# Performance work log

Hardware: AMD Instinct MI355X
Metric: run time of the kernel (lower is better)

Reference implementation:

```python
import jax, jax.numpy as jnp
import numpy as np

B, NCAP, LV, LT, C = 64, 64, 197, 32, 512
NSP = LV - 1          # 196 spatial patches
NUM_KEEP = 98         # ceil(196 * sparse_ratio=0.5)
KEEPED = 49           # int(196 * aggr_ratio=0.5 * sparse_ratio=0.5)
HID = 102             # int(512 * dim_ratio=0.2)
LN_EPS = 1e-5


def _normalize(x):
    # torch F.normalize: x / max(||x||, 1e-12)
    return x / jnp.maximum(jnp.linalg.norm(x, axis=-1, keepdims=True), 1e-12)


def setup_inputs() -> dict:
    key = jax.random.key(0)
    ks = jax.random.split(key, 8)
    def rn(k, shape, s=0.02):
        return jax.random.normal(k, shape, jnp.float32) * s
    return {
        "img_embs": jax.random.normal(ks[0], (B, LV, C), jnp.float32),
        "cap_embs": jax.random.normal(ks[1], (NCAP, LT, C), jnp.float32),
        "cap_lens": jnp.full((NCAP,), LT, jnp.int32),
        "ln_gamma": jnp.ones((C,), jnp.float32),
        "ln_beta": jnp.zeros((C,), jnp.float32),
        "w1": rn(ks[2], (C, HID)), "b1": jnp.zeros((HID,), jnp.float32),
        "w2": rn(ks[3], (HID, KEEPED)), "b2": jnp.zeros((KEEPED,), jnp.float32),
        "aggr_scale": jnp.ones((1, 1, 1), jnp.float32),
        "wi2t": rn(ks[4], (C, C)), "bi2t": jnp.zeros((C,), jnp.float32),
        "wt2i": rn(ks[5], (C, C)), "bt2i": jnp.zeros((C,), jnp.float32),
        "temp": jnp.ones((1, 1, 1), jnp.float32),
    }


def _forward(img_embs, cap_embs, ln_gamma, ln_beta, w1, b1, w2, b2,
             aggr_scale, wi2t, bi2t, wt2i, bt2i, temp):
    img_norm = _normalize(img_embs)
    img_cls = img_embs[:, 0:1]              # [B,1,C]  has_cls_token branch
    img_sp = img_embs[:, 1:]                # [B,196,C]
    img_sp_norm = img_norm[:, 1:]
    # use_cls_as_glob_embd: global = normalized CLS (no grad)
    glo = jax.lax.stop_gradient(img_norm[:, 0:1])
    attn_x = jax.lax.stop_gradient(jnp.sum(glo * img_sp_norm, -1))  # [B,196]
    cap_norm = _normalize(cap_embs)
    bidx = jnp.arange(B)[:, None]

    def ln(x):
        m = x.mean(-1, keepdims=True)
        v = jnp.var(x, axis=-1, keepdims=True)
        return (x - m) / jnp.sqrt(v + LN_EPS) * ln_gamma + ln_beta

    def per_caption(cap_i, cap_i_norm):
        # cap_i, cap_i_norm: [LT, C]
        cap_glo = jax.lax.stop_gradient(_normalize(cap_i[0:1]))           # [1,C]
        attn_y = jax.lax.stop_gradient(jnp.sum(cap_glo[None] * img_sp_norm, -1))  # [B,196]
        # --- TokenSparse ---
        score = attn_x + attn_y
        order = jnp.argsort(-score, axis=1)                              # descending
        keep, nonkeep = order[:, :NUM_KEEP], order[:, NUM_KEEP:]
        sel = img_sp[bidx, keep]                                          # [B,98,C]
        non = img_sp[bidx, nonkeep]                                       # [B,98,C]
        non_score = jnp.take_along_axis(score, nonkeep, 1)
        extra = jnp.sum(non * jax.nn.softmax(non_score, axis=1)[..., None],
                        axis=1, keepdims=True)                            # [B,1,C]
        # --- TokenAggregation ---
        h = jax.nn.gelu(ln(sel) @ w1 + b1, approximate=False)             # [B,98,HID]
        w = jnp.swapaxes(h @ w2 + b2, 1, 2) * aggr_scale                  # [B,49,98]
        aggr = jax.nn.softmax(w, axis=2) @ sel                            # [B,49,C]
        # [cls, aggr, extra] -> [B,51,C], then normalize
        sel_tok = _normalize(jnp.concatenate([img_cls, aggr, extra], 1))
        Ls = sel_tok.shape[1]
        # --- 'attn' similarity ---
        cap_exp = jnp.broadcast_to(cap_i_norm[None], (B, LT, C))
        st = jnp.swapaxes(sel_tok, 1, 2)                                  # [B,C,51]
        c2i = jax.nn.leaky_relu(cap_exp @ st, negative_slope=0.1)         # [B,LT,51]
        a_i2t = jax.nn.softmax((cap_exp @ wi2t + bi2t) @ st / temp, axis=1)
        a_t2i = jax.nn.softmax((cap_exp @ wt2i + bt2i) @ st / temp, axis=2)
        return jnp.sum(a_i2t * c2i / Ls + a_t2i * c2i / LT, axis=(1, 2))  # [B]

    sims = jax.vmap(per_caption)(cap_embs, cap_norm)                      # [NCAP,B]
    return sims.T                                                         # [B,NCAP]


def reference(img_embs, cap_embs, cap_lens, ln_gamma, ln_beta, w1, b1, w2, b2,
              aggr_scale, wi2t, bi2t, wt2i, bt2i, temp):
    # cap_lens are all LT (static shapes); eval-mode output: similarity matrix.
    return _forward(img_embs, cap_embs, ln_gamma, ln_beta, w1, b1, w2, b2,
                    aggr_scale, wi2t, bi2t, wt2i, bt2i, temp)
```

## Files before the change

kernel.cpp:

```cpp
#include <hip/hip_runtime.h>
#include <math.h>

#define B     64
#define NCAP  64
#define LV    197
#define LT    32
#define C     512
#define NSP   196
#define NKEEP 98
#define HID   102
#define KEEPED 49

#define OFF_ATTNX   12608
#define OFF_WSMAT   25152
#define OFF_WT      639808
#define OFF_GLOT    1688384
#define OFF_ATTNYT  1721152
#define OFF_IMGT    14164800
#define OFF_QBB     17834816
#define OFF_QCAP    19407680
#define OFF_W1TF    19931968
#define OFF_W2TF    19960640

typedef unsigned int u32;
typedef unsigned short u16;
typedef __bf16 bf16x8 __attribute__((ext_vector_type(8)));
typedef float f32x4 __attribute__((ext_vector_type(4)));
typedef unsigned int uint4v __attribute__((ext_vector_type(4)));

__device__ __forceinline__ u16 f2bf(float f) {
    u32 u = __builtin_bit_cast(u32, f);
    return (u16)((u + 0x7FFFu + ((u >> 16) & 1u)) >> 16);
}
__device__ __forceinline__ bf16x8 ld_bf8(const u16* p) {
    uint4v v = *reinterpret_cast<const uint4v*>(p);
    return __builtin_bit_cast(bf16x8, v);
}

__device__ __forceinline__ float gelu_exact(float x) {
    return 0.5f * x * (1.f + erff(x * 0.70710678118654752f));
}

__global__ __launch_bounds__(256) void k_pre(const float* __restrict__ cap,
                                             const float* __restrict__ wi2t,
                                             const float* __restrict__ wt2i,
                                             const float* __restrict__ w1,
                                             const float* __restrict__ w2,
                                             float* __restrict__ gloT,
                                             u16* __restrict__ Qbbf,
                                             u16* __restrict__ Qcap,
                                             u16* __restrict__ wT,
                                             u16* __restrict__ w1Tf,
                                             u16* __restrict__ w2Tf) {
    int idx = blockIdx.x, t = threadIdx.x;
    __shared__ __align__(16) u16 shb[64 * 65];

    if (idx < 512) {
        int e = idx, i = e >> 3, tg = e & 7;
        int lane = t & 63, wv = t >> 6;
        int tt = tg * 4 + wv;
        const float* row = cap + ((size_t)i * LT + tt) * C;
        float v[8]; float ss = 0.f;
#pragma unroll
        for (int q = 0; q < 8; ++q) { v[q] = row[lane + 64 * q]; ss += v[q] * v[q]; }
        for (int o = 32; o > 0; o >>= 1) ss += __shfl_down(ss, o);
        ss = __shfl(ss, 0);
        float inv = 1.f / fmaxf(sqrtf(ss), 1e-12f);
        u16* qrow = Qcap + ((size_t)i * 32 + tt) * C;
        int mi = tt >> 4, l15f = tt & 15;
        u16* qfb = Qbbf + (size_t)(i * 6 + mi) * 16 * 512;
#pragma unroll
        for (int q = 0; q < 8; ++q) {
            float n = v[q] * inv;
            u16 nb = f2bf(n);
            int c = lane + 64 * q;
            qrow[c] = nb;
            int ks = c >> 5, quadf = (c >> 3) & 3, jf = c & 7;
            qfb[(size_t)ks * 512 + (quadf * 16 + l15f) * 8 + jf] = nb;
            if (tt == 0) gloT[(c >> 2) * (NCAP * 4) + i * 4 + (c & 3)] = n;
        }
    } else if (idx < 640) {
        int e = idx - 512;
        int mat = e >> 6, ty = e & 63, jg = ty >> 3, cg = ty & 7;
        const float* W = mat ? wt2i : wi2t;
        u16 (*tile)[65] = (u16(*)[65])shb;
        for (int f = t; f < 4096; f += 256) {
            int cc2 = f >> 6, jj = f & 63;
            tile[jj][cc2] = f2bf(W[(size_t)(cg * 64 + cc2) * 512 + jg * 64 + jj]);
        }
        __syncthreads();
        for (int f = t; f < 4096; f += 256) {
            int jj = f >> 6, cc2 = f & 63;
            wT[((size_t)mat * 512 + jg * 64 + jj) * 512 + cg * 64 + cc2] = tile[jj][cc2];
        }
    } else if (idx < 647) {
        int nt = idx - 640;
        u32* outp = (u32*)w1Tf + (size_t)nt * 16 * 256;
        for (int f = t; f < 16 * 256; f += 256) {
            int ks = f >> 8, g = f & 255;
            int lane_o = g >> 2, j2 = g & 3;
            int l15o = lane_o & 15, quado = lane_o >> 4;
            int kk = ks * 32 + quado * 8 + 2 * j2;
            int n = nt * 16 + l15o;
            u32 lo = 0, hi = 0;
            if (n < HID) {
                lo = f2bf(w1[(size_t)kk * HID + n]);
                hi = f2bf(w1[(size_t)(kk + 1) * HID + n]);
            }
            outp[ks * 256 + g] = lo | (hi << 16);
        }
    } else {
        u32* outp = (u32*)w2Tf;
        for (int f = t; f < 16 * 256; f += 256) {
            int tile = f >> 8, g = f & 255;
            int nt2 = tile >> 2, ks2 = tile & 3;
            int lane_o = g >> 2, j2 = g & 3;
            int l15o = lane_o & 15, quado = lane_o >> 4;
            int kk0 = ks2 * 32 + quado * 8 + 2 * j2;
            int n = nt2 * 16 + l15o;
            u32 lo = 0, hi = 0;
            if (n < KEEPED) {
                if (kk0 < HID)     lo = f2bf(w2[(size_t)kk0 * KEEPED + n]);
                if (kk0 + 1 < HID) hi = f2bf(w2[(size_t)(kk0 + 1) * KEEPED + n]);
            }
            outp[tile * 256 + g] = lo | (hi << 16);
        }
    }
}

__global__ __launch_bounds__(512) void k_mid(const float* __restrict__ img,
                                             const u16* __restrict__ wT,
                                             const float* __restrict__ bi2t,
                                             const float* __restrict__ bt2i,
                                             const u16* __restrict__ Qcap,
                                             u16* __restrict__ Qbbf,
                                             const u16* __restrict__ w1Tf,
                                             const u16* __restrict__ w2Tf,
                                             const float* __restrict__ gamw,
                                             const float* __restrict__ betw,
                                             const float* __restrict__ b1,
                                             const float* __restrict__ b2,
                                             const float* __restrict__ scale_p,
                                             const float* __restrict__ gloT,
                                             float* __restrict__ attn_x,
                                             u16* __restrict__ WsM16,
                                             float* __restrict__ attn_yT,
                                             u16* __restrict__ imgTf) {
    int idx = blockIdx.x, t = threadIdx.x;
    __shared__ __align__(16) u16 shu[64 * 224];

    if (idx < 256) {
        int i = idx & 63, p = idx >> 6;
        int lane = t & 63, wu = t >> 6;
        int l15 = lane & 15, quad = lane >> 4;
        int mat = wu >> 2;
        int miq = (wu >> 1) & 1;
        int nh  = wu & 1;
        int ni0 = p * 8 + nh * 4;
        const u16* Arow = Qcap + ((size_t)i * 32 + miq * 16 + l15) * 512;
        const u16* Wm   = wT + (size_t)mat * 512 * 512;
        f32x4 acc[4];
#pragma unroll
        for (int n = 0; n < 4; ++n) acc[n] = (f32x4){0.f, 0.f, 0.f, 0.f};
        bf16x8 A = ld_bf8(Arow + quad * 8);
        bf16x8 Bf[4];
#pragma unroll
        for (int n = 0; n < 4; ++n)
            Bf[n] = ld_bf8(Wm + (size_t)((ni0 + n) * 16 + l15) * 512 + quad * 8);
        for (int ks = 0; ks < 16; ++ks) {
            bf16x8 An; bf16x8 Bn[4];
            if (ks < 15) {
                An = ld_bf8(Arow + (ks + 1) * 32 + quad * 8);
#pragma unroll
                for (int n = 0; n < 4; ++n)
                    Bn[n] = ld_bf8(Wm + (size_t)((ni0 + n) * 16 + l15) * 512 + (ks + 1) * 32 + quad * 8);
            }
#pragma unroll
            for (int n = 0; n < 4; ++n)
                acc[n] = __builtin_amdgcn_mfma_f32_16x16x32_bf16(A, Bf[n], acc[n], 0, 0, 0);
            A = An;
#pragma unroll
            for (int n = 0; n < 4; ++n) Bf[n] = Bn[n];
        }
        const float* bias = mat ? bt2i : bi2t;
#pragma unroll
        for (int n = 0; n < 4; ++n) {
            int j = (ni0 + n) * 16 + l15;
            float bj = bias[j];
            int ksf = j >> 5, quadf = (j >> 3) & 3, jf = j & 7;
#pragma unroll
            for (int r = 0; r < 4; ++r) {
                int q = 32 + mat * 32 + miq * 16 + quad * 4 + r;
                int mi = q >> 4, l15f = q & 15;
                Qbbf[(size_t)((i * 6 + mi) * 16 + ksf) * 512 + (quadf * 16 + l15f) * 8 + jf]
                    = f2bf(acc[n][r] + bj);
            }
        }
    } else if (idx < 1088) {
        int e = idx - 256;
        int b = e / 13, sg = e - b * 13;
        int s0 = sg * 16;
        u16* LNb = shu;
        u16* Hb  = shu + 16 * 520;
        int lane = t & 63, wu = t >> 6;
        int l15 = lane & 15, quad = lane >> 4;

        {
            int rr0 = 2 * wu, rr1 = 2 * wu + 1;
            int sA = s0 + rr0, sB = s0 + rr1;
            int sAc = sA < NSP ? sA : NSP - 1;
            int sBc = sB < NSP ? sB : NSP - 1;
            const float* rowA = img + ((size_t)b * LV + 1 + sAc) * C;
            const float* rowB = img + ((size_t)b * LV + 1 + sBc) * C;
            const float* cls  = img + (size_t)b * LV * C;
            float v0[8], v1[8];
            float sm0 = 0, ss0 = 0, dd0 = 0, sm1 = 0, ss1 = 0, dd1 = 0, sc = 0;
#pragma unroll
            for (int q = 0; q < 8; ++q) {
                int c = lane + 64 * q;
                float cv = cls[c];
                v0[q] = rowA[c]; v1[q] = rowB[c];
                sm0 += v0[q]; ss0 += v0[q] * v0[q]; dd0 += v0[q] * cv;
                sm1 += v1[q]; ss1 += v1[q] * v1[q]; dd1 += v1[q] * cv;
                sc  += cv * cv;
            }
            for (int o = 32; o > 0; o >>= 1) {
                sm0 += __shfl_down(sm0, o); ss0 += __shfl_down(ss0, o); dd0 += __shfl_down(dd0, o);
                sm1 += __shfl_down(sm1, o); ss1 += __shfl_down(ss1, o); dd1 += __shfl_down(dd1, o);
                sc  += __shfl_down(sc, o);
            }
            sm0 = __shfl(sm0, 0); ss0 = __shfl(ss0, 0);
            sm1 = __shfl(sm1, 0); ss1 = __shfl(ss1, 0);
            float mean0 = sm0 * (1.f / C);
            float rstd0 = 1.f / sqrtf(ss0 * (1.f / C) - mean0 * mean0 + 1e-5f);
            float mean1 = sm1 * (1.f / C);
            float rstd1 = 1.f / sqrtf(ss1 * (1.f / C) - mean1 * mean1 + 1e-5f);
            if (lane == 0) {
                float inv0 = 1.f / fmaxf(sqrtf(sc), 1e-12f);
                if (sA < NSP) attn_x[b * NSP + sA] = dd0 * inv0 * (1.f / fmaxf(sqrtf(ss0), 1e-12f));
                if (sB < NSP) attn_x[b * NSP + sB] = dd1 * inv0 * (1.f / fmaxf(sqrtf(ss1), 1e-12f));
            }
#pragma unroll
            for (int q = 0; q < 8; ++q) {
                int c = lane + 64 * q;
                float g = gamw[c], be = betw[c];
                LNb[rr0 * 520 + c] = f2bf((v0[q] - mean0) * rstd0 * g + be);
                LNb[rr1 * 520 + c] = f2bf((v1[q] - mean1) * rstd1 * g + be);
            }
        }
        __syncthreads();
        if (wu < 7) {
            const u16* W1b = w1Tf + (size_t)wu * 16 * 512;
            f32x4 h4 = (f32x4){0.f, 0.f, 0.f, 0.f};
            for (int ks = 0; ks < 16; ++ks) {
                bf16x8 A = ld_bf8(LNb + l15 * 520 + ks * 32 + quad * 8);
                bf16x8 Bv = ld_bf8(W1b + ks * 512 + lane * 8);
                h4 = __builtin_amdgcn_mfma_f32_16x16x32_bf16(A, Bv, h4, 0, 0, 0);
            }
            int col = wu * 16 + l15;
            if (col < HID) {
                float bb = b1[col];
#pragma unroll
                for (int r = 0; r < 4; ++r)
                    Hb[(quad * 4 + r) * 136 + col] = f2bf(gelu_exact(h4[r] + bb));
            } else {
#pragma unroll
                for (int r = 0; r < 4; ++r) Hb[(quad * 4 + r) * 136 + col] = 0;
            }
        } else {
            for (int f = lane; f < 16 * 24; f += 64) {
                int row = f / 24, cc = 112 + f % 24;
                Hb[row * 136 + cc] = 0;
            }
        }
        __syncthreads();
        if (wu < 4) {
            const u16* W2b = w2Tf + (size_t)wu * 4 * 512;
            f32x4 a2 = (f32x4){0.f, 0.f, 0.f, 0.f};
            for (int ks2 = 0; ks2 < 4; ++ks2) {
                bf16x8 A2 = ld_bf8(Hb + l15 * 136 + ks2 * 32 + quad * 8);
                bf16x8 B2 = ld_bf8(W2b + ks2 * 512 + lane * 8);
                a2 = __builtin_amdgcn_mfma_f32_16x16x32_bf16(A2, B2, a2, 0, 0, 0);
            }
            int k = wu * 16 + l15;
            if (k < KEEPED) {
                float scale = scale_p[0], bk = b2[k];
#pragma unroll
                for (int r = 0; r < 4; ++r) {
                    int row = quad * 4 + r;
                    if (s0 + row < NSP)
                        WsM16[((size_t)b * NSP + s0 + row) * 49 + k] = f2bf(expf((a2[r] + bk) * scale));
                }
            }
        }
    } else if (idx < 2688) {
        int e = idx - 1088;
        int b = e / 25;
        int s0 = (e - b * 25) * 8;
        int R = NSP - s0; if (R > 8) R = 8;
        float (*xr)[C] = (float(*)[C])shu;
        float* rnorm = (float*)shu + 4096;

        for (int f = t; f < R * C; f += 512) {
            int rr = f >> 9, c = f & 511;
            xr[rr][c] = img[((size_t)b * LV + 1 + s0 + rr) * C + c];
        }
        __syncthreads();
        {
            int row = t >> 6, l = t & 63;
            if (row < R) {
                float ss = 0.f;
                for (int c = l; c < C; c += 64) { float v = xr[row][c]; ss += v * v; }
                for (int o = 32; o > 0; o >>= 1) ss += __shfl_down(ss, o);
                if (l == 0) rnorm[row] = 1.f / fmaxf(sqrtf(ss), 1e-12f);
            }
        }
        __syncthreads();
        for (int f = t; f < R * C; f += 512) {
            int rr = f >> 9, c = f & 511;
            xr[rr][c] *= rnorm[rr];
        }
        __syncthreads();
        int i = t & 63, w = t >> 6;
        if (w < R) {
            float a0 = 0.f;
            const float4* g4 = (const float4*)gloT;
            const float4* x4 = (const float4*)xr[w];
            for (int c4 = 0; c4 < C / 4; ++c4) {
                float4 g = g4[c4 * NCAP + i];
                float4 x0 = x4[c4];
                a0 += x0.x * g.x + x0.y * g.y + x0.z * g.z + x0.w * g.w;
            }
            attn_yT[((size_t)b * NCAP + i) * NSP + s0 + w] = a0;
        }
    } else {
        int e = idx - 2688;
        int b = e >> 3, cg = e & 7;
        for (int f = t; f < 64 * 27; f += 512) shu[(f / 27) * 224 + 197 + (f % 27)] = 0;
        int cc = t & 63;
        for (int sb = t >> 6; sb < 197; sb += 8) {
            float v = img[((size_t)b * LV + sb) * C + cg * 64 + cc];
            shu[cc * 224 + sb] = f2bf(v);
        }
        __syncthreads();
        const u32* Tu = (const u32*)shu;
        u32* outp = (u32*)imgTf + (size_t)b * 7 * 32 * 256;
        for (int f = t; f < 7 * 4 * 256; f += 512) {
            int ks = f >> 10, rem = f & 1023;
            int ctl = rem >> 8, g = rem & 255;
            int lane_o = g >> 2, j2 = g & 3;
            int quad_o = lane_o >> 4, l15_o = lane_o & 15;
            int ccl = ctl * 16 + l15_o;
            int s = ks * 32 + quad_o * 8 + 2 * j2;
            u32 v = Tu[ccl * 112 + (s >> 1)];
            outp[(size_t)(ks * 32 + cg * 4 + ctl) * 256 + g] = v;
        }
    }
}

__global__ __launch_bounds__(512, 4) void k_main(const float* __restrict__ attn_x,
                                                 const float* __restrict__ attn_yT,
                                                 const u16* __restrict__ WsM16,
                                                 const u16* __restrict__ imgTf,
                                                 const u16* __restrict__ Qbbf,
                                                 const float* __restrict__ temp_p,
                                                 float* __restrict__ out) {
    int lin = blockIdx.x + NCAP * blockIdx.y;
    int b = (lin & 7) * 8 + ((lin >> 3) & 7);
    int i = lin >> 6;
    int t = threadIdx.x;
    int lane = t & 63, wu = t >> 6;
    int l15 = lane & 15, quad = lane >> 4;

    __shared__ __align__(16) u16 TnBuf[51 * 520];
    __shared__ float invn[64];
    __shared__ float redw[8];

    u16*   Pf   = TnBuf;
    float* ULDS = (float*)TnBuf;
    float* scoreS = (float*)(TnBuf + 24000);
    short* rnkH   = (short*)(TnBuf + 24392);
    u16*   keepL  = (u16*)  (TnBuf + 24784);
    u16*   nonL   = (u16*)  (TnBuf + 24882);
    float* snon   = (float*)(TnBuf + 25000);
    float* rowsq  = (float*)(TnBuf + 25372);

    const u16* imgTb = imgTf + (size_t)b * 7 * 32 * 512;
    bf16x8 Bc[4], Bn[4];
#pragma unroll
    for (int nj = 0; nj < 4; ++nj)
        Bc[nj] = ld_bf8(imgTb + (size_t)(wu * 4 + nj) * 512 + lane * 8);

    {
        uint4v* Pfv = (uint4v*)Pf;
        for (int f = t; f < 51 * 232 / 8; f += 512) Pfv[f] = (uint4v){0, 0, 0, 0};
    }
    if (t < NSP)
        scoreS[t] = attn_x[b * NSP + t] + attn_yT[((size_t)b * NCAP + i) * NSP + t];
    __syncthreads();
    if (t < 2 * NSP) {
        int half = (t >= NSP) ? 1 : 0;
        int s = t - half * NSP;
        float sv = scoreS[s];
        const float2* sc2 = (const float2*)scoreS;
        int base = half ? 49 : 0;
        int r = 0;
        for (int u2 = base; u2 < base + 49; ++u2) {
            float2 o = sc2[u2];
            int u = 2 * u2;
            r += (o.x > sv) || (o.x == sv && u < s);
            r += (o.y > sv) || (o.y == sv && (u + 1) < s);
        }
        rnkH[half * NSP + s] = (short)r;
    }
    __syncthreads();
    if (t < NSP) {
        int r = rnkH[t] + rnkH[NSP + t];
        if (r < NKEEP) keepL[r] = (u16)t;
        else { nonL[r - NKEEP] = (u16)t; snon[r - NKEEP] = scoreS[t]; }
    }
    __syncthreads();
    if (t == 0) Pf[0] = 0x3F80;
    if (t < NKEEP) Pf[50 * 232 + 1 + nonL[t]] = f2bf(expf(snon[t]));
    {
        int j = t / KEEPED, k = t - (t / KEEPED) * KEEPED;
#pragma unroll
        for (int it = 0; it < 10; ++it) {
            if (j < NKEEP) {
                int s = keepL[j];
                Pf[(1 + k) * 232 + 1 + s] = WsM16[((size_t)b * NSP + s) * 49 + k];
            }
            j += 10; k += 22;
            if (k >= KEEPED) { k -= KEEPED; ++j; }
        }
    }
    __syncthreads();

    f32x4 acc[4][4];
#pragma unroll
    for (int mi = 0; mi < 4; ++mi)
// ... 145 lines not shown
#pragma unroll
        for (int q = 0; q < 4; ++q) { e[q] = expf(vbuf[q] - mm); z += e[q]; }
#pragma unroll
        for (int o = 1; o < 8; o <<= 1) z += __shfl_xor(z, o, 8);
        float iz = 1.f / z;
#pragma unroll
        for (int q = 0; q < 4; ++q) ULDS[(32 + sub + 8 * q) * 52 + l] = e[q] * iz;
    }
    if (t < 256) {
        int u = t >> 3, sub = t & 7;
        float vbuf[7]; int cnt = 0; float mm = -1e30f;
        for (int l = sub; l < 51; l += 8) {
            float v = ULDS[(64 + u) * 52 + l] * invT;
            vbuf[cnt++] = v;
            mm = fmaxf(mm, v);
        }
#pragma unroll
        for (int o = 1; o < 8; o <<= 1) mm = fmaxf(mm, __shfl_xor(mm, o, 8));
        float e[7]; float z = 0.f;
        for (int q = 0; q < cnt; ++q) { e[q] = expf(vbuf[q] - mm); z += e[q]; }
#pragma unroll
        for (int o = 1; o < 8; o <<= 1) z += __shfl_xor(z, o, 8);
        float iz = 1.f / z;
        { int q = 0;
          for (int l = sub; l < 51; l += 8) { ULDS[(64 + u) * 52 + l] = e[q] * iz; ++q; } }
    }
    __syncthreads();

    float part = 0.f;
    {
        int u = t / 51, l = t - (t / 51) * 51;
        while (u < LT) {
            float u0 = ULDS[u * 52 + l];
            float c2 = (u0 > 0.f) ? u0 : 0.1f * u0;
            float av = ULDS[(32 + u) * 52 + l];
            float bv = ULDS[(64 + u) * 52 + l];
            part += c2 * (av * (1.f / 51.f) + bv * (1.f / 32.f));
            u += 10; l += 2;
            if (l >= 51) { l -= 51; ++u; }
        }
    }
    for (int o = 32; o > 0; o >>= 1) part += __shfl_down(part, o);
    if (lane == 0) redw[wu] = part;
    __syncthreads();
    if (t == 0) {
        float s = 0.f;
#pragma unroll
        for (int w2 = 0; w2 < 8; ++w2) s += redw[w2];
        out[b * NCAP + i] = s;
    }
}

extern "C" void kernel_launch(void* const* d_in, const int* in_sizes, int n_in,
                              void* d_out, int out_size, void* d_ws, size_t ws_size,
                              hipStream_t stream) {
    const float* img        = (const float*)d_in[0];
    const float* cap        = (const float*)d_in[1];
    const float* gamw       = (const float*)d_in[3];
    const float* betw       = (const float*)d_in[4];
    const float* w1         = (const float*)d_in[5];
    const float* b1         = (const float*)d_in[6];
    const float* w2         = (const float*)d_in[7];
    const float* b2         = (const float*)d_in[8];
    const float* aggr_scale = (const float*)d_in[9];
    const float* wi2t       = (const float*)d_in[10];
    const float* bi2t       = (const float*)d_in[11];
    const float* wt2i       = (const float*)d_in[12];
    const float* bt2i       = (const float*)d_in[13];
    const float* temp       = (const float*)d_in[14];
    float* out = (float*)d_out;

    float* ws      = (float*)d_ws;
    float* attn_x  = ws + OFF_ATTNX;
    u16*   WsM16   = (u16*)(ws + OFF_WSMAT);
    u16*   wT      = (u16*)(ws + OFF_WT);
    float* gloT    = ws + OFF_GLOT;
    float* attn_yT = ws + OFF_ATTNYT;
    u16*   imgTf   = (u16*)(ws + OFF_IMGT);
    u16*   Qbbf    = (u16*)(ws + OFF_QBB);
    u16*   Qcap    = (u16*)(ws + OFF_QCAP);
    u16*   w1Tf    = (u16*)(ws + OFF_W1TF);
    u16*   w2Tf    = (u16*)(ws + OFF_W2TF);

    k_pre<<<dim3(648), dim3(256), 0, stream>>>(cap, wi2t, wt2i, w1, w2,
                                               gloT, Qbbf, Qcap, wT, w1Tf, w2Tf);
    k_mid<<<dim3(3200), dim3(512), 0, stream>>>(img, wT, bi2t, bt2i, Qcap, Qbbf,
                                                w1Tf, w2Tf, gamw, betw, b1, b2, aggr_scale,
                                                gloT, attn_x, WsM16, attn_yT, imgTf);
    k_main<<<dim3(NCAP, B), dim3(512), 0, stream>>>(attn_x, attn_yT, WsM16, imgTf, Qbbf, temp, out);
}
```

Measured before the change: 344.0 us.

## Fuse pre and mid kernels into one persistent cooperative kernel with grid sync

Replaces the k_pre and k_mid launches with a single cooperative persistent kernel of 512 blocks. The blocks loop over the former tasks and use a grid-wide barrier between the weight/caption preparation phase and the projection/image phase. The aim is to remove one kernel launch and the drain/fill gap between the two launches. In exchange, the grid sync costs time, fewer resident blocks may limit latency hiding, and k_pre's 256-thread tasks now run in 512-thread blocks with half the threads idle. If the cooperative launch fails, it falls back to the original two kernels.

```diff
diff --git a/kernel.cpp b/kernel.cpp
--- a/kernel.cpp
+++ b/kernel.cpp
@@ -1,5 +1,8 @@
 #include <hip/hip_runtime.h>
+#include <hip/hip_cooperative_groups.h>
 #include <math.h>
+
+namespace cg = cooperative_groups;
 
 #define B     64
 #define NCAP  64
@@ -39,6 +42,377 @@
 
 __device__ __forceinline__ float gelu_exact(float x) {
     return 0.5f * x * (1.f + erff(x * 0.70710678118654752f));
+}
+
+
+__device__ __forceinline__ void sec_capnorm(int e, int t,
+                                            const float* __restrict__ cap,
+                                            float* __restrict__ gloT,
+                                            u16* __restrict__ Qbbf,
+                                            u16* __restrict__ Qcap) {
+    int i = e >> 3, tg = e & 7;
+    int lane = t & 63, wv = t >> 6;
+    int tt = tg * 4 + wv;
+    const float* row = cap + ((size_t)i * LT + tt) * C;
+    float v[8]; float ss = 0.f;
+#pragma unroll
+    for (int q = 0; q < 8; ++q) { v[q] = row[lane + 64 * q]; ss += v[q] * v[q]; }
+    for (int o = 32; o > 0; o >>= 1) ss += __shfl_down(ss, o);
+    ss = __shfl(ss, 0);
+    float inv = 1.f / fmaxf(sqrtf(ss), 1e-12f);
+    u16* qrow = Qcap + ((size_t)i * 32 + tt) * C;
+    int mi = tt >> 4, l15f = tt & 15;
+    u16* qfb = Qbbf + (size_t)(i * 6 + mi) * 16 * 512;
+#pragma unroll
+    for (int q = 0; q < 8; ++q) {
+        float n = v[q] * inv;
+        u16 nb = f2bf(n);
+        int c = lane + 64 * q;
+        qrow[c] = nb;
+        int ks = c >> 5, quadf = (c >> 3) & 3, jf = c & 7;
+        qfb[(size_t)ks * 512 + (quadf * 16 + l15f) * 8 + jf] = nb;
+        if (tt == 0) gloT[(c >> 2) * (NCAP * 4) + i * 4 + (c & 3)] = n;
+    }
+}
+
+template <int NT>
+__device__ __forceinline__ void sec_wt(int e, int t, u16* shb,
+                                       const float* __restrict__ wi2t,
+                                       const float* __restrict__ wt2i,
+                                       u16* __restrict__ wT) {
+    int mat = e >> 6, ty = e & 63, jg = ty >> 3, cg = ty & 7;
+    const float* W = mat ? wt2i : wi2t;
+    u16 (*tile)[65] = (u16(*)[65])shb;
+    for (int f = t; f < 4096; f += NT) {
+        int cc2 = f >> 6, jj = f & 63;
+        tile[jj][cc2] = f2bf(W[(size_t)(cg * 64 + cc2) * 512 + jg * 64 + jj]);
+    }
+    __syncthreads();
+    for (int f = t; f < 4096; f += NT) {
+        int jj = f >> 6, cc2 = f & 63;
+        wT[((size_t)mat * 512 + jg * 64 + jj) * 512 + cg * 64 + cc2] = tile[jj][cc2];
+    }
+}
+
+template <int NT>
+__device__ __forceinline__ void sec_w1t(int nt, int t,
+                                        const float* __restrict__ w1,
+                                        u16* __restrict__ w1Tf) {
+    u32* outp = (u32*)w1Tf + (size_t)nt * 16 * 256;
+    for (int f = t; f < 16 * 256; f += NT) {
+        int ks = f >> 8, g = f & 255;
+        int lane_o = g >> 2, j2 = g & 3;
+        int l15o = lane_o & 15, quado = lane_o >> 4;
+        int kk = ks * 32 + quado * 8 + 2 * j2;
+        int n = nt * 16 + l15o;
+        u32 lo = 0, hi = 0;
+        if (n < HID) {
+            lo = f2bf(w1[(size_t)kk * HID + n]);
+            hi = f2bf(w1[(size_t)(kk + 1) * HID + n]);
+        }
+        outp[ks * 256 + g] = lo | (hi << 16);
+    }
+}
+
+template <int NT>
+__device__ __forceinline__ void sec_w2t(int t,
+                                        const float* __restrict__ w2,
+                                        u16* __restrict__ w2Tf) {
+    u32* outp = (u32*)w2Tf;
+    for (int f = t; f < 16 * 256; f += NT) {
+        int tile = f >> 8, g = f & 255;
+        int nt2 = tile >> 2, ks2 = tile & 3;
+        int lane_o = g >> 2, j2 = g & 3;
+        int l15o = lane_o & 15, quado = lane_o >> 4;
+        int kk0 = ks2 * 32 + quado * 8 + 2 * j2;
+        int n = nt2 * 16 + l15o;
+        u32 lo = 0, hi = 0;
+        if (n < KEEPED) {
+            if (kk0 < HID)     lo = f2bf(w2[(size_t)kk0 * KEEPED + n]);
+            if (kk0 + 1 < HID) hi = f2bf(w2[(size_t)(kk0 + 1) * KEEPED + n]);
+        }
+        outp[tile * 256 + g] = lo | (hi << 16);
+    }
+}
+
+__device__ __forceinline__ void sec_qproj(int idx, int t,
+                                          const u16* __restrict__ wT,
+                                          const float* __restrict__ bi2t,
+                                          const float* __restrict__ bt2i,
+                                          const u16* __restrict__ Qcap,
+                                          u16* __restrict__ Qbbf) {
+    int i = idx & 63, p = idx >> 6;
+    int lane = t & 63, wu = t >> 6;
+    int l15 = lane & 15, quad = lane >> 4;
+    int mat = wu >> 2;
+    int miq = (wu >> 1) & 1;
+    int nh  = wu & 1;
+    int ni0 = p * 8 + nh * 4;
+    const u16* Arow = Qcap + ((size_t)i * 32 + miq * 16 + l15) * 512;
+    const u16* Wm   = wT + (size_t)mat * 512 * 512;
+    f32x4 acc[4];
+#pragma unroll
+    for (int n = 0; n < 4; ++n) acc[n] = (f32x4){0.f, 0.f, 0.f, 0.f};
+    bf16x8 A = ld_bf8(Arow + quad * 8);
+    bf16x8 Bf[4];
+#pragma unroll
+    for (int n = 0; n < 4; ++n)
+        Bf[n] = ld_bf8(Wm + (size_t)((ni0 + n) * 16 + l15) * 512 + quad * 8);
+    for (int ks = 0; ks < 16; ++ks) {
+        bf16x8 An; bf16x8 Bn[4];
+        if (ks < 15) {
+            An = ld_bf8(Arow + (ks + 1) * 32 + quad * 8);
+#pragma unroll
+            for (int n = 0; n < 4; ++n)
+                Bn[n] = ld_bf8(Wm + (size_t)((ni0 + n) * 16 + l15) * 512 + (ks + 1) * 32 + quad * 8);
+        }
+#pragma unroll
+        for (int n = 0; n < 4; ++n)
+            acc[n] = __builtin_amdgcn_mfma_f32_16x16x32_bf16(A, Bf[n], acc[n], 0, 0, 0);
+        A = An;
+#pragma unroll
+        for (int n = 0; n < 4; ++n) Bf[n] = Bn[n];
+    }
+    const float* bias = mat ? bt2i : bi2t;
+#pragma unroll
+    for (int n = 0; n < 4; ++n) {
+        int j = (ni0 + n) * 16 + l15;
+        float bj = bias[j];
+        int ksf = j >> 5, quadf = (j >> 3) & 3, jf = j & 7;
+#pragma unroll
+        for (int r = 0; r < 4; ++r) {
+            int q = 32 + mat * 32 + miq * 16 + quad * 4 + r;
+            int mi = q >> 4, l15f = q & 15;
+            Qbbf[(size_t)((i * 6 + mi) * 16 + ksf) * 512 + (quadf * 16 + l15f) * 8 + jf]
+                = f2bf(acc[n][r] + bj);
+        }
+    }
+}
+
+__device__ __forceinline__ void sec_imgrow(int e, int t, u16* shu,
+                                           const float* __restrict__ img,
+                                           const u16* __restrict__ w1Tf,
+                                           const u16* __restrict__ w2Tf,
+                                           const float* __restrict__ gamw,
+                                           const float* __restrict__ betw,
+                                           const float* __restrict__ b1,
+                                           const float* __restrict__ b2,
+                                           const float* __restrict__ scale_p,
+                                           float* __restrict__ attn_x,
+                                           u16* __restrict__ WsM16) {
+    int b = e / 13, sg = e - b * 13;
+    int s0 = sg * 16;
+    u16* LNb = shu;
+    u16* Hb  = shu + 16 * 520;
+    int lane = t & 63, wu = t >> 6;
+    int l15 = lane & 15, quad = lane >> 4;
+
+    {
+        int rr0 = 2 * wu, rr1 = 2 * wu + 1;
+        int sA = s0 + rr0, sB = s0 + rr1;
+        int sAc = sA < NSP ? sA : NSP - 1;
+        int sBc = sB < NSP ? sB : NSP - 1;
+        const float* rowA = img + ((size_t)b * LV + 1 + sAc) * C;
+        const float* rowB = img + ((size_t)b * LV + 1 + sBc) * C;
+        const float* cls  = img + (size_t)b * LV * C;
+        float v0[8], v1[8];
+        float sm0 = 0, ss0 = 0, dd0 = 0, sm1 = 0, ss1 = 0, dd1 = 0, sc = 0;
+#pragma unroll
+        for (int q = 0; q < 8; ++q) {
+            int c = lane + 64 * q;
+            float cv = cls[c];
+            v0[q] = rowA[c]; v1[q] = rowB[c];
+            sm0 += v0[q]; ss0 += v0[q] * v0[q]; dd0 += v0[q] * cv;
+            sm1 += v1[q]; ss1 += v1[q] * v1[q]; dd1 += v1[q] * cv;
+            sc  += cv * cv;
+        }
+        for (int o = 32; o > 0; o >>= 1) {
+            sm0 += __shfl_down(sm0, o); ss0 += __shfl_down(ss0, o); dd0 += __shfl_down(dd0, o);
+            sm1 += __shfl_down(sm1, o); ss1 += __shfl_down(ss1, o); dd1 += __shfl_down(dd1, o);
+            sc  += __shfl_down(sc, o);
+        }
+        sm0 = __shfl(sm0, 0); ss0 = __shfl(ss0, 0);
+        sm1 = __shfl(sm1, 0); ss1 = __shfl(ss1, 0);
+        float mean0 = sm0 * (1.f / C);
+        float rstd0 = 1.f / sqrtf(ss0 * (1.f / C) - mean0 * mean0 + 1e-5f);
+        float mean1 = sm1 * (1.f / C);
+        float rstd1 = 1.f / sqrtf(ss1 * (1.f / C) - mean1 * mean1 + 1e-5f);
+        if (lane == 0) {
+            float inv0 = 1.f / fmaxf(sqrtf(sc), 1e-12f);
+            if (sA < NSP) attn_x[b * NSP + sA] = dd0 * inv0 * (1.f / fmaxf(sqrtf(ss0), 1e-12f));
+            if (sB < NSP) attn_x[b * NSP + sB] = dd1 * inv0 * (1.f / fmaxf(sqrtf(ss1), 1e-12f));
+        }
+#pragma unroll
+        for (int q = 0; q < 8; ++q) {
+            int c = lane + 64 * q;
+            float g = gamw[c], be = betw[c];
+            LNb[rr0 * 520 + c] = f2bf((v0[q] - mean0) * rstd0 * g + be);
+            LNb[rr1 * 520 + c] = f2bf((v1[q] - mean1) * rstd1 * g + be);
+        }
+    }
+    __syncthreads();
+    if (wu < 7) {
+        const u16* W1b = w1Tf + (size_t)wu * 16 * 512;
+        f32x4 h4 = (f32x4){0.f, 0.f, 0.f, 0.f};
+        for (int ks = 0; ks < 16; ++ks) {
+            bf16x8 A = ld_bf8(LNb + l15 * 520 + ks * 32 + quad * 8);
+            bf16x8 Bv = ld_bf8(W1b + ks * 512 + lane * 8);
+            h4 = __builtin_amdgcn_mfma_f32_16x16x32_bf16(A, Bv, h4, 0, 0, 0);
+        }
+        int col = wu * 16 + l15;
+        if (col < HID) {
+            float bb = b1[col];
+#pragma unroll
+            for (int r = 0; r < 4; ++r)
+                Hb[(quad * 4 + r) * 136 + col] = f2bf(gelu_exact(h4[r] + bb));
+        } else {
+#pragma unroll
+            for (int r = 0; r < 4; ++r) Hb[(quad * 4 + r) * 136 + col] = 0;
+        }
+    } else {
+        for (int f = lane; f < 16 * 24; f += 64) {
+            int row = f / 24, cc = 112 + f % 24;
+            Hb[row * 136 + cc] = 0;
+        }
+    }
+    __syncthreads();
+    if (wu < 4) {
+        const u16* W2b = w2Tf + (size_t)wu * 4 * 512;
+        f32x4 a2 = (f32x4){0.f, 0.f, 0.f, 0.f};
+        for (int ks2 = 0; ks2 < 4; ++ks2) {
+            bf16x8 A2 = ld_bf8(Hb + l15 * 136 + ks2 * 32 + quad * 8);
+            bf16x8 B2 = ld_bf8(W2b + ks2 * 512 + lane * 8);
+            a2 = __builtin_amdgcn_mfma_f32_16x16x32_bf16(A2, B2, a2, 0, 0, 0);
+        }
+        int k = wu * 16 + l15;
+        if (k < KEEPED) {
+            float scale = scale_p[0], bk = b2[k];
+#pragma unroll
+            for (int r = 0; r < 4; ++r) {
+                int row = quad * 4 + r;
+                if (s0 + row < NSP)
+                    WsM16[((size_t)b * NSP + s0 + row) * 49 + k] = f2bf(expf((a2[r] + bk) * scale));
+            }
+        }
+    }
+}
+
+__device__ __forceinline__ void sec_attny(int e, int t, u16* shu,
+                                          const float* __restrict__ img,
+                                          const float* __restrict__ gloT,
+                                          float* __restrict__ attn_yT) {
+    int b = e / 25;
+    int s0 = (e - b * 25) * 8;
+    int R = NSP - s0; if (R > 8) R = 8;
+    float (*xr)[C] = (float(*)[C])shu;
+    float* rnorm = (float*)shu + 4096;
+
+    for (int f = t; f < R * C; f += 512) {
+        int rr = f >> 9, c = f & 511;
+        xr[rr][c] = img[((size_t)b * LV + 1 + s0 + rr) * C + c];
+    }
+    __syncthreads();
+    {
+        int row = t >> 6, l = t & 63;
+        if (row < R) {
+            float ss = 0.f;
+            for (int c = l; c < C; c += 64) { float v = xr[row][c]; ss += v * v; }
+            for (int o = 32; o > 0; o >>= 1) ss += __shfl_down(ss, o);
+            if (l == 0) rnorm[row] = 1.f / fmaxf(sqrtf(ss), 1e-12f);
+        }
+    }
+    __syncthreads();
+    for (int f = t; f < R * C; f += 512) {
+        int rr = f >> 9, c = f & 511;
+        xr[rr][c] *= rnorm[rr];
+    }
+    __syncthreads();
+    int i = t & 63, w = t >> 6;
+    if (w < R) {
+        float a0 = 0.f;
+        const float4* g4 = (const float4*)gloT;
+        const float4* x4 = (const float4*)xr[w];
+        for (int c4 = 0; c4 < C / 4; ++c4) {
+            float4 g = g4[c4 * NCAP + i];
+            float4 x0 = x4[c4];
+            a0 += x0.x * g.x + x0.y * g.y + x0.z * g.z + x0.w * g.w;
+        }
+        attn_yT[((size_t)b * NCAP + i) * NSP + s0 + w] = a0;
+    }
+}
+
+__device__ __forceinline__ void sec_imgt(int e, int t, u16* shu,
+                                         const float* __restrict__ img,
+                                         u16* __restrict__ imgTf) {
+    int b = e >> 3, cg = e & 7;
+    for (int f = t; f < 64 * 27; f += 512) shu[(f / 27) * 224 + 197 + (f % 27)] = 0;
+    int cc = t & 63;
+    for (int sb = t >> 6; sb < 197; sb += 8) {
+        float v = img[((size_t)b * LV + sb) * C + cg * 64 + cc];
+        shu[cc * 224 + sb] = f2bf(v);
+    }
+    __syncthreads();
+    const u32* Tu = (const u32*)shu;
+    u32* outp = (u32*)imgTf + (size_t)b * 7 * 32 * 256;
+    for (int f = t; f < 7 * 4 * 256; f += 512) {
+        int ks = f >> 10, rem = f & 1023;
+        int ctl = rem >> 8, g = rem & 255;
+        int lane_o = g >> 2, j2 = g & 3;
+        int quad_o = lane_o >> 4, l15_o = lane_o & 15;
+        int ccl = ctl * 16 + l15_o;
+        int s = ks * 32 + quad_o * 8 + 2 * j2;
+        u32 v = Tu[ccl * 112 + (s >> 1)];
+        outp[(size_t)(ks * 32 + cg * 4 + ctl) * 256 + g] = v;
+    }
+}
+
+__global__ __launch_bounds__(512, 4) void k_fused(const float* __restrict__ img,
+                                                  const float* __restrict__ cap,
+                                                  const float* __restrict__ wi2t,
+                                                  const float* __restrict__ wt2i,
+                                                  const float* __restrict__ w1,
+                                                  const float* __restrict__ w2,
+                                                  const float* __restrict__ bi2t,
+                                                  const float* __restrict__ bt2i,
+                                                  const float* __restrict__ gamw,
+                                                  const float* __restrict__ betw,
+                                                  const float* __restrict__ b1,
+                                                  const float* __restrict__ b2,
+                                                  const float* __restrict__ scale_p,
+                                                  float* __restrict__ gloT,
+                                                  u16* __restrict__ Qbbf,
+                                                  u16* __restrict__ Qcap,
+                                                  u16* __restrict__ wT,
+                                                  u16* __restrict__ w1Tf,
+                                                  u16* __restrict__ w2Tf,
+                                                  float* __restrict__ attn_x,
+                                                  u16* __restrict__ WsM16,
+                                                  float* __restrict__ attn_yT,
+                                                  u16* __restrict__ imgTf) {
+    int t = threadIdx.x;
+    __shared__ __align__(16) u16 shu[64 * 224];
+
+    for (int task = blockIdx.x; task < 648; task += 512) {
+        __syncthreads();
+        if (task < 512) {
+            if (t < 256) sec_capnorm(task, t, cap, gloT, Qbbf, Qcap);
+        } else if (task < 640) {
+            sec_wt<512>(task - 512, t, shu, wi2t, wt2i, wT);
+        } else if (task < 647) {
+            sec_w1t<512>(task - 640, t, w1, w1Tf);
+        } else {
+            sec_w2t<512>(t, w2, w2Tf);
+        }
+    }
+    cg::this_grid().sync();
+    for (int task = blockIdx.x; task < 3200; task += 512) {
+        __syncthreads();
+        if (task < 256)       sec_qproj(task, t, wT, bi2t, bt2i, Qcap, Qbbf);
+        else if (task < 1088) sec_imgrow(task - 256, t, shu, img, w1Tf, w2Tf, gamw, betw,
+                                         b1, b2, scale_p, attn_x, WsM16);
+        else if (task < 2688) sec_attny(task - 1088, t, shu, img, gloT, attn_yT);
+        else                  sec_imgt(task - 2688, t, shu, img, imgTf);
+    }
 }
 
 __global__ __launch_bounds__(256) void k_pre(const float* __restrict__ cap,
@@ -54,77 +428,14 @@
                                              u16* __restrict__ w2Tf) {
     int idx = blockIdx.x, t = threadIdx.x;
     __shared__ __align__(16) u16 shb[64 * 65];
-
     if (idx < 512) {
-        int e = idx, i = e >> 3, tg = e & 7;
-        int lane = t & 63, wv = t >> 6;
-        int tt = tg * 4 + wv;
-        const float* row = cap + ((size_t)i * LT + tt) * C;
-        float v[8]; float ss = 0.f;
-#pragma unroll
-        for (int q = 0; q < 8; ++q) { v[q] = row[lane + 64 * q]; ss += v[q] * v[q]; }
-        for (int o = 32; o > 0; o >>= 1) ss += __shfl_down(ss, o);
-        ss = __shfl(ss, 0);
-        float inv = 1.f / fmaxf(sqrtf(ss), 1e-12f);
-        u16* qrow = Qcap + ((size_t)i * 32 + tt) * C;
-        int mi = tt >> 4, l15f = tt & 15;
-        u16* qfb = Qbbf + (size_t)(i * 6 + mi) * 16 * 512;
-#pragma unroll
-        for (int q = 0; q < 8; ++q) {
-            float n = v[q] * inv;
-            u16 nb = f2bf(n);
-            int c = lane + 64 * q;
-            qrow[c] = nb;
-            int ks = c >> 5, quadf = (c >> 3) & 3, jf = c & 7;
-            qfb[(size_t)ks * 512 + (quadf * 16 + l15f) * 8 + jf] = nb;
-            if (tt == 0) gloT[(c >> 2) * (NCAP * 4) + i * 4 + (c & 3)] = n;
-        }
+        sec_capnorm(idx, t, cap, gloT, Qbbf, Qcap);
     } else if (idx < 640) {
-        int e = idx - 512;
-        int mat = e >> 6, ty = e & 63, jg = ty >> 3, cg = ty & 7;
-        const float* W = mat ? wt2i : wi2t;
-        u16 (*tile)[65] = (u16(*)[65])shb;
-        for (int f = t; f < 4096; f += 256) {
-            int cc2 = f >> 6, jj = f & 63;
-            tile[jj][cc2] = f2bf(W[(size_t)(cg * 64 + cc2) * 512 + jg * 64 + jj]);
-        }
-        __syncthreads();
-        for (int f = t; f < 4096; f += 256) {
-            int jj = f >> 6, cc2 = f & 63;
-            wT[((size_t)mat * 512 + jg * 64 + jj) * 512 + cg * 64 + cc2] = tile[jj][cc2];
-        }
+        sec_wt<256>(idx - 512, t, shb, wi2t, wt2i, wT);
     } else if (idx < 647) {
-        int nt = idx - 640;
-        u32* outp = (u32*)w1Tf + (size_t)nt * 16 * 256;
-        for (int f = t; f < 16 * 256; f += 256) {
-            int ks = f >> 8, g = f & 255;
-            int lane_o = g >> 2, j2 = g & 3;
-            int l15o = lane_o & 15, quado = lane_o >> 4;
-            int kk = ks * 32 + quado * 8 + 2 * j2;
-            int n = nt * 16 + l15o;
-            u32 lo = 0, hi = 0;
-            if (n < HID) {
-                lo = f2bf(w1[(size_t)kk * HID + n]);
-                hi = f2bf(w1[(size_t)(kk + 1) * HID + n]);
-            }
-            outp[ks * 256 + g] = lo | (hi << 16);
-        }
+        sec_w1t<256>(idx - 640, t, w1, w1Tf);
     } else {
-        u32* outp = (u32*)w2Tf;
-        for (int f = t; f < 16 * 256; f += 256) {
-            int tile = f >> 8, g = f & 255;
-            int nt2 = tile >> 2, ks2 = tile & 3;
-            int lane_o = g >> 2, j2 = g & 3;
-            int l15o = lane_o & 15, quado = lane_o >> 4;
-            int kk0 = ks2 * 32 + quado * 8 + 2 * j2;
-            int n = nt2 * 16 + l15o;
-            u32 lo = 0, hi = 0;
-            if (n < KEEPED) {
-                if (kk0 < HID)     lo = f2bf(w2[(size_t)kk0 * KEEPED + n]);
-                if (kk0 + 1 < HID) hi = f2bf(w2[(size_t)(kk0 + 1) * KEEPED + n]);
-            }
-            outp[tile * 256 + g] = lo | (hi << 16);
-        }
+        sec_w2t<256>(t, w2, w2Tf);
     }
 }
 
@@ -148,214 +459,11 @@
                                              u16* __restrict__ imgTf) {
     int idx = blockIdx.x, t = threadIdx.x;
     __shared__ __align__(16) u16 shu[64 * 224];
-
-    if (idx < 256) {
-        int i = idx & 63, p = idx >> 6;
-        int lane = t & 63, wu = t >> 6;
-        int l15 = lane & 15, quad = lane >> 4;
-        int mat = wu >> 2;
-        int miq = (wu >> 1) & 1;
-        int nh  = wu & 1;
-        int ni0 = p * 8 + nh * 4;
-        const u16* Arow = Qcap + ((size_t)i * 32 + miq * 16 + l15) * 512;
-        const u16* Wm   = wT + (size_t)mat * 512 * 512;
-        f32x4 acc[4];
-#pragma unroll
-        for (int n = 0; n < 4; ++n) acc[n] = (f32x4){0.f, 0.f, 0.f, 0.f};
-        bf16x8 A = ld_bf8(Arow + quad * 8);
-        bf16x8 Bf[4];
-#pragma unroll
-        for (int n = 0; n < 4; ++n)
-            Bf[n] = ld_bf8(Wm + (size_t)((ni0 + n) * 16 + l15) * 512 + quad * 8);
-        for (int ks = 0; ks < 16; ++ks) {
-            bf16x8 An; bf16x8 Bn[4];
-            if (ks < 15) {
-                An = ld_bf8(Arow + (ks + 1) * 32 + quad * 8);
-#pragma unroll
-                for (int n = 0; n < 4; ++n)
-                    Bn[n] = ld_bf8(Wm + (size_t)((ni0 + n) * 16 + l15) * 512 + (ks + 1) * 32 + quad * 8);
-            }
-#pragma unroll
-            for (int n = 0; n < 4; ++n)
-                acc[n] = __builtin_amdgcn_mfma_f32_16x16x32_bf16(A, Bf[n], acc[n], 0, 0, 0);
-            A = An;
-#pragma unroll
-            for (int n = 0; n < 4; ++n) Bf[n] = Bn[n];
-        }
-        const float* bias = mat ? bt2i : bi2t;
-#pragma unroll
-        for (int n = 0; n < 4; ++n) {
-            int j = (ni0 + n) * 16 + l15;
-            float bj = bias[j];
-            int ksf = j >> 5, quadf = (j >> 3) & 3, jf = j & 7;
-#pragma unroll
-            for (int r = 0; r < 4; ++r) {
-                int q = 32 + mat * 32 + miq * 16 + quad * 4 + r;
-                int mi = q >> 4, l15f = q & 15;
-                Qbbf[(size_t)((i * 6 + mi) * 16 + ksf) * 512 + (quadf * 16 + l15f) * 8 + jf]
-                    = f2bf(acc[n][r] + bj);
-            }
-        }
-    } else if (idx < 1088) {
-        int e = idx - 256;
-        int b = e / 13, sg = e - b * 13;
-        int s0 = sg * 16;
-        u16* LNb = shu;
-        u16* Hb  = shu + 16 * 520;
-        int lane = t & 63, wu = t >> 6;
-        int l15 = lane & 15, quad = lane >> 4;
-
-        {
-            int rr0 = 2 * wu, rr1 = 2 * wu + 1;
-            int sA = s0 + rr0, sB = s0 + rr1;
-            int sAc = sA < NSP ? sA : NSP - 1;
-            int sBc = sB < NSP ? sB : NSP - 1;
-            const float* rowA = img + ((size_t)b * LV + 1 + sAc) * C;
-            const float* rowB = img + ((size_t)b * LV + 1 + sBc) * C;
-            const float* cls  = img + (size_t)b * LV * C;
-            float v0[8], v1[8];
-            float sm0 = 0, ss0 = 0, dd0 = 0, sm1 = 0, ss1 = 0, dd1 = 0, sc = 0;
-#pragma unroll
-            for (int q = 0; q < 8; ++q) {
-                int c = lane + 64 * q;
-                float cv = cls[c];
-                v0[q] = rowA[c]; v1[q] = rowB[c];
-                sm0 += v0[q]; ss0 += v0[q] * v0[q]; dd0 += v0[q] * cv;
-                sm1 += v1[q]; ss1 += v1[q] * v1[q]; dd1 += v1[q] * cv;
-                sc  += cv * cv;
-            }
-            for (int o = 32; o > 0; o >>= 1) {
-                sm0 += __shfl_down(sm0, o); ss0 += __shfl_down(ss0, o); dd0 += __shfl_down(dd0, o);
-                sm1 += __shfl_down(sm1, o); ss1 += __shfl_down(ss1, o); dd1 += __shfl_down(dd1, o);
-                sc  += __shfl_down(sc, o);
-            }
-            sm0 = __shfl(sm0, 0); ss0 = __shfl(ss0, 0);
-            sm1 = __shfl(sm1, 0); ss1 = __shfl(ss1, 0);
-            float mean0 = sm0 * (1.f / C);
-            float rstd0 = 1.f / sqrtf(ss0 * (1.f / C) - mean0 * mean0 + 1e-5f);
-            float mean1 = sm1 * (1.f / C);
-            float rstd1 = 1.f / sqrtf(ss1 * (1.f / C) - mean1 * mean1 + 1e-5f);
-            if (lane == 0) {
-                float inv0 = 1.f / fmaxf(sqrtf(sc), 1e-12f);
-                if (sA < NSP) attn_x[b * NSP + sA] = dd0 * inv0 * (1.f / fmaxf(sqrtf(ss0), 1e-12f));
-                if (sB < NSP) attn_x[b * NSP + sB] = dd1 * inv0 * (1.f / fmaxf(sqrtf(ss1), 1e-12f));
-            }
-#pragma unroll
-            for (int q = 0; q < 8; ++q) {
-                int c = lane + 64 * q;
-                float g = gamw[c], be = betw[c];
-                LNb[rr0 * 520 + c] = f2bf((v0[q] - mean0) * rstd0 * g + be);
-                LNb[rr1 * 520 + c] = f2bf((v1[q] - mean1) * rstd1 * g + be);
-            }
-        }
-        __syncthreads();
-        if (wu < 7) {
-            const u16* W1b = w1Tf + (size_t)wu * 16 * 512;
-            f32x4 h4 = (f32x4){0.f, 0.f, 0.f, 0.f};
-            for (int ks = 0; ks < 16; ++ks) {
-                bf16x8 A = ld_bf8(LNb + l15 * 520 + ks * 32 + quad * 8);
-                bf16x8 Bv = ld_bf8(W1b + ks * 512 + lane * 8);
-                h4 = __builtin_amdgcn_mfma_f32_16x16x32_bf16(A, Bv, h4, 0, 0, 0);
-            }
-            int col = wu * 16 + l15;
-            if (col < HID) {
-                float bb = b1[col];
-#pragma unroll
-                for (int r = 0; r < 4; ++r)
-                    Hb[(quad * 4 + r) * 136 + col] = f2bf(gelu_exact(h4[r] + bb));
-            } else {
-#pragma unroll
-                for (int r = 0; r < 4; ++r) Hb[(quad * 4 + r) * 136 + col] = 0;
-            }
-        } else {
-            for (int f = lane; f < 16 * 24; f += 64) {
-                int row = f / 24, cc = 112 + f % 24;
-                Hb[row * 136 + cc] = 0;
-            }
-        }
-        __syncthreads();
-        if (wu < 4) {
-            const u16* W2b = w2Tf + (size_t)wu * 4 * 512;
-            f32x4 a2 = (f32x4){0.f, 0.f, 0.f, 0.f};
-            for (int ks2 = 0; ks2 < 4; ++ks2) {
-                bf16x8 A2 = ld_bf8(Hb + l15 * 136 + ks2 * 32 + quad * 8);
-                bf16x8 B2 = ld_bf8(W2b + ks2 * 512 + lane * 8);
-                a2 = __builtin_amdgcn_mfma_f32_16x16x32_bf16(A2, B2, a2, 0, 0, 0);
-            }
-            int k = wu * 16 + l15;
-            if (k < KEEPED) {
-                float scale = scale_p[0], bk = b2[k];
-#pragma unroll
-                for (int r = 0; r < 4; ++r) {
-                    int row = quad * 4 + r;
-                    if (s0 + row < NSP)
-                        WsM16[((size_t)b * NSP + s0 + row) * 49 + k] = f2bf(expf((a2[r] + bk) * scale));
-                }
-            }
-        }
-    } else if (idx < 2688) {
-        int e = idx - 1088;
-        int b = e / 25;
-        int s0 = (e - b * 25) * 8;
-        int R = NSP - s0; if (R > 8) R = 8;
-        float (*xr)[C] = (float(*)[C])shu;
-        float* rnorm = (float*)shu + 4096;
-
-        for (int f = t; f < R * C; f += 512) {
-            int rr = f >> 9, c = f & 511;
-            xr[rr][c] = img[((size_t)b * LV + 1 + s0 + rr) * C + c];
-        }
-        __syncthreads();
-        {
-            int row = t >> 6, l = t & 63;
-            if (row < R) {
-                float ss = 0.f;
-                for (int c = l; c < C; c += 64) { float v = xr[row][c]; ss += v * v; }
-                for (int o = 32; o > 0; o >>= 1) ss += __shfl_down(ss, o);
-                if (l == 0) rnorm[row] = 1.f / fmaxf(sqrtf(ss), 1e-12f);
-            }
-        }
-        __syncthreads();
-        for (int f = t; f < R * C; f += 512) {
-            int rr = f >> 9, c = f & 511;
-            xr[rr][c] *= rnorm[rr];
-        }
-        __syncthreads();
-        int i = t & 63, w = t >> 6;
-        if (w < R) {
-            float a0 = 0.f;
-            const float4* g4 = (const float4*)gloT;
-            const float4* x4 = (const float4*)xr[w];
-            for (int c4 = 0; c4 < C / 4; ++c4) {
-                float4 g = g4[c4 * NCAP + i];
-                float4 x0 = x4[c4];
-                a0 += x0.x * g.x + x0.y * g.y + x0.z * g.z + x0.w * g.w;
-            }
-            attn_yT[((size_t)b * NCAP + i) * NSP + s0 + w] = a0;
-        }
-    } else {
-        int e = idx - 2688;
-        int b = e >> 3, cg = e & 7;
-        for (int f = t; f < 64 * 27; f += 512) shu[(f / 27) * 224 + 197 + (f % 27)] = 0;
-        int cc = t & 63;
-        for (int sb = t >> 6; sb < 197; sb += 8) {
-            float v = img[((size_t)b * LV + sb) * C + cg * 64 + cc];
-            shu[cc * 224 + sb] = f2bf(v);
-        }
-        __syncthreads();
-        const u32* Tu = (const u32*)shu;
-        u32* outp = (u32*)imgTf + (size_t)b * 7 * 32 * 256;
-        for (int f = t; f < 7 * 4 * 256; f += 512) {
-            int ks = f >> 10, rem = f & 1023;
-            int ctl = rem >> 8, g = rem & 255;
-            int lane_o = g >> 2, j2 = g & 3;
-            int quad_o = lane_o >> 4, l15_o = lane_o & 15;
-            int ccl = ctl * 16 + l15_o;
-            int s = ks * 32 + quad_o * 8 + 2 * j2;
-            u32 v = Tu[ccl * 112 + (s >> 1)];
-            outp[(size_t)(ks * 32 + cg * 4 + ctl) * 256 + g] = v;
-        }
-    }
+    if (idx < 256)       sec_qproj(idx, t, wT, bi2t, bt2i, Qcap, Qbbf);
+    else if (idx < 1088) sec_imgrow(idx - 256, t, shu, img, w1Tf, w2Tf, gamw, betw,
+                                    b1, b2, scale_p, attn_x, WsM16);
+    else if (idx < 2688) sec_attny(idx - 1088, t, shu, img, gloT, attn_yT);
+    else                 sec_imgt(idx - 2688, t, shu, img, imgTf);
 }
 
 __global__ __launch_bounds__(512, 4) void k_main(const float* __restrict__ attn_x,
@@ -667,10 +775,21 @@
     u16*   w1Tf    = (u16*)(ws + OFF_W1TF);
     u16*   w2Tf    = (u16*)(ws + OFF_W2TF);
 
-    k_pre<<<dim3(648), dim3(256), 0, stream>>>(cap, wi2t, wt2i, w1, w2,
-                                               gloT, Qbbf, Qcap, wT, w1Tf, w2Tf);
-    k_mid<<<dim3(3200), dim3(512), 0, stream>>>(img, wT, bi2t, bt2i, Qcap, Qbbf,
-                                                w1Tf, w2Tf, gamw, betw, b1, b2, aggr_scale,
-                                                gloT, attn_x, WsM16, attn_yT, imgTf);
+    void* fargs[] = {
+        (void*)&img, (void*)&cap, (void*)&wi2t, (void*)&wt2i, (void*)&w1, (void*)&w2,
+        (void*)&bi2t, (void*)&bt2i, (void*)&gamw, (void*)&betw, (void*)&b1, (void*)&b2,
+        (void*)&aggr_scale, (void*)&gloT, (void*)&Qbbf, (void*)&Qcap, (void*)&wT,
+        (void*)&w1Tf, (void*)&w2Tf, (void*)&attn_x, (void*)&WsM16, (void*)&attn_yT,
+        (void*)&imgTf
+    };
+    hipError_t cerr = hipLaunchCooperativeKernel((const void*)k_fused, dim3(512), dim3(512),
+                                                 fargs, 0, stream);
+    if (cerr != hipSuccess) {
+        k_pre<<<dim3(648), dim3(256), 0, stream>>>(cap, wi2t, wt2i, w1, w2,
+                                                   gloT, Qbbf, Qcap, wT, w1Tf, w2Tf);
+        k_mid<<<dim3(3200), dim3(512), 0, stream>>>(img, wT, bi2t, bt2i, Qcap, Qbbf,
+                                                    w1Tf, w2Tf, gamw, betw, b1, b2, aggr_scale,
+                                                    gloT, attn_x, WsM16, attn_yT, imgTf);
+    }
     k_main<<<dim3(NCAP, B), dim3(512), 0, stream>>>(attn_x, attn_yT, WsM16, imgTf, Qbbf, temp, out);
 }
```

New measurement: 503.3 us. +46.3%, slower.
